# Performance work log

Measured on AMD Instinct MI355X. Metric: run time of the kernel, lower is better.

## Reference

```python
import jax, jax.numpy as jnp
import numpy as np

N_NODES = 100000
IN_CH = 256
H1, C1 = 8, 8   # conv1: heads=8, out_channels=8
H2, C2 = 1, 3   # conv2: heads=1, out_channels=3
NEG_SLOPE = 0.2
EPS = 1e-16


def gat_conv(x, src, dst, W, a_src, a_dst, b, heads, out_ch, n_nodes):
    """PyG-style GATConv (eval mode, self-loops already in src/dst)."""
    h = (x @ W).reshape(n_nodes, heads, out_ch)          # [N,H,C]
    alpha_s = jnp.einsum('nhc,hc->nh', h, a_src)         # [N,H]
    alpha_d = jnp.einsum('nhc,hc->nh', h, a_dst)         # [N,H]
    e = alpha_s[src] + alpha_d[dst]                      # [E,H]
    e = jnp.where(e > 0, e, NEG_SLOPE * e)               # leaky_relu(0.2)
    # segment softmax over destination nodes
    m = jax.ops.segment_max(e, dst, num_segments=n_nodes)
    m = jnp.where(jnp.isfinite(m), m, 0.0)
    ex = jnp.exp(e - m[dst])
    s = jax.ops.segment_sum(ex, dst, num_segments=n_nodes)
    a = ex / (s[dst] + EPS)                              # [E,H]
    msg = h[src] * a[:, :, None]                         # [E,H,C]
    out = jax.ops.segment_sum(msg, dst, num_segments=n_nodes)  # [N,H,C]
    return out.reshape(n_nodes, heads * out_ch) + b


def setup_inputs() -> dict:
    key = jax.random.key(0)
    ks = jax.random.split(key, 10)
    x = jax.random.normal(ks[0], (N_NODES, IN_CH), dtype=jnp.float32)
    edge_index = jax.random.randint(ks[1], (2, 3200000), 0, N_NODES, dtype=jnp.int64)
    sc = 0.1
    return {
        'x': x,
        'edge_index': edge_index,
        'W1': jax.random.normal(ks[2], (IN_CH, H1 * C1), dtype=jnp.float32) * sc,
        'a_src1': jax.random.normal(ks[3], (H1, C1), dtype=jnp.float32) * sc,
        'a_dst1': jax.random.normal(ks[4], (H1, C1), dtype=jnp.float32) * sc,
        'b1': jnp.zeros((H1 * C1,), dtype=jnp.float32),
        'W2': jax.random.normal(ks[5], (H1 * C1, H2 * C2), dtype=jnp.float32) * sc,
        'a_src2': jax.random.normal(ks[6], (H2, C2), dtype=jnp.float32) * sc,
        'a_dst2': jax.random.normal(ks[7], (H2, C2), dtype=jnp.float32) * sc,
        'b2': jnp.zeros((H2 * C2,), dtype=jnp.float32),
    }


def reference(x, edge_index, W1, a_src1, a_dst1, b1, W2, a_src2, a_dst2, b2):
    n = x.shape[0]
    loop = jnp.arange(n, dtype=edge_index.dtype)
    src = jnp.concatenate([edge_index[0], loop])  # add_self_loops=True
    dst = jnp.concatenate([edge_index[1], loop])
    h = gat_conv(x, src, dst, W1, a_src1, a_dst1, b1, H1, C1, n)
    h = jax.nn.elu(h)
    out = gat_conv(h, src, dst, W2, a_src2, a_dst2, b2, H2, C2, n)
    return out
```

## Files before the change

### kernel.cpp

```cpp
#include <hip/hip_runtime.h>
#include <hip/hip_bf16.h>

#define P_W1  0
#define P_AS1 16384
#define P_AD1 16448
#define P_B1  16512
#define P_W2  16576
#define P_AS2 16768
#define P_AD2 16771
#define P_B2  16774

typedef __attribute__((ext_vector_type(8))) short short8;
typedef __attribute__((ext_vector_type(4))) float floatx4;

__device__ __forceinline__ float ldf(const void* p, int i, int bf) {
  if (bf) {
    unsigned v = ((unsigned)((const unsigned short*)p)[i]) << 16;
    float f; __builtin_memcpy(&f, &v, 4); return f;
  }
  return ((const float*)p)[i];
}
__device__ __forceinline__ int ldi(const void* p, long i, int i64) {
  return i64 ? ((const int*)p)[2*i] : ((const int*)p)[i];
}
__device__ __forceinline__ unsigned short f2bfbits(float f) {
  __hip_bfloat16 b = __float2bfloat16(f);
  unsigned short u; __builtin_memcpy(&u, &b, 2); return u;
}

__global__ void k_prep(const void* x, const void* ei,
                       const void* w1, const void* as1, const void* ad1, const void* b1,
                       const void* w2, const void* as2, const void* ad2, const void* b2,
                       int* flags, float* params, unsigned short* w1t) {
  __shared__ int sh[2];
  int tid = threadIdx.x, lane = tid & 63, w = tid >> 6;
  if (w == 0) {
    const unsigned* xw = (const unsigned*)x;
    int hits = 0;
    for (int i = lane; i < 256; i += 64) {
      unsigned b = (xw[i] >> 7) & 0xFF;
      hits += (b >= 96 && b <= 141) ? 1 : 0;
    }
    for (int o = 32; o >= 1; o >>= 1) hits += __shfl_xor(hits, o);
    if (lane == 0) sh[0] = (hits >= 160) ? 1 : 0;
  } else if (w == 1) {
    const unsigned* ew = (const unsigned*)ei;
    int z = 0;
    for (int i = lane; i < 128; i += 64) z += (ew[2*i+1] == 0u) ? 1 : 0;
    for (int o = 32; o >= 1; o >>= 1) z += __shfl_xor(z, o);
    if (lane == 0) sh[1] = (z >= 64) ? 1 : 0;
  }
  __syncthreads();
  int bf = sh[0];
  if (tid == 0) { flags[0] = sh[0]; flags[1] = sh[1]; }
  for (int i = tid; i < 16384; i += blockDim.x) {
    int ch = i >> 8, k = i & 255;
    w1t[i] = f2bfbits(ldf(w1, k * 64 + ch, bf));
  }
  if (!bf) {
    for (int i = tid; i < 16384; i += blockDim.x) params[P_W1 + i] = ldf(w1, i, bf);
  }
  for (int i = tid; i < 64; i += blockDim.x) {
    params[P_AS1 + i] = ldf(as1, i, bf);
    params[P_AD1 + i] = ldf(ad1, i, bf);
    params[P_B1  + i] = ldf(b1,  i, bf);
  }
  for (int i = tid; i < 192; i += blockDim.x) params[P_W2 + i] = ldf(w2, i, bf);
  for (int i = tid; i < 3; i += blockDim.x) {
    params[P_AS2 + i] = ldf(as2, i, bf);
    params[P_AD2 + i] = ldf(ad2, i, bf);
    params[P_B2  + i] = ldf(b2,  i, bf);
  }
}

#define XP 272

__device__ __forceinline__ void gemm1_f32(const float* x, const float* params,
                                          float* h1, float* a_s, float* a_d,
                                          int N, int wave, int lane) {
  int n0 = wave * 4;
  if (n0 >= N) return;
  int nb[4];
#pragma unroll
  for (int j = 0; j < 4; j++) nb[j] = min(n0 + j, N - 1) * 256;
  float acc[4] = {0.f, 0.f, 0.f, 0.f};
  const float* W = params + P_W1;
  for (int k = 0; k < 256; k++) {
    float wv = W[k * 64 + lane];
#pragma unroll
    for (int j = 0; j < 4; j++) acc[j] += x[nb[j] + k] * wv;
  }
  float as1v = params[P_AS1 + lane], ad1v = params[P_AD1 + lane];
#pragma unroll
  for (int j = 0; j < 4; j++) {
    int n = n0 + j;
    if (n >= N) break;
    float hv = acc[j];
    float s = hv * as1v, d = hv * ad1v;
    s += __shfl_xor(s, 1); s += __shfl_xor(s, 2); s += __shfl_xor(s, 4);
    d += __shfl_xor(d, 1); d += __shfl_xor(d, 2); d += __shfl_xor(d, 4);
    h1[(size_t)n * 64 + lane] = hv;
    if ((lane & 7) == 0) {
      a_s[n * 8 + (lane >> 3)] = s;
      a_d[n * 8 + (lane >> 3)] = d;
    }
  }
}

__global__ void k_gemm1(const void* x, const unsigned short* w1t, const int* flags,
                        const float* params, float* h1, float* a_s, float* a_d, int N) {
  __shared__ unsigned short xs[16 * XP];
  int tid = threadIdx.x;
  int wv = tid >> 6, lane = tid & 63;
  if (flags[0]) {
    const unsigned short* xb = (const unsigned short*)x;
    int n0 = blockIdx.x * 16;
#pragma unroll
    for (int it = 0; it < 2; it++) {
      int idx = tid + it * 256;
      int row = idx >> 5, col = idx & 31;
      int gn = n0 + row; if (gn >= N) gn = N - 1;
      uint4 v = *(const uint4*)(xb + (size_t)gn * 256 + col * 8);
      *(uint4*)(xs + row * XP + col * 8) = v;
    }
    __syncthreads();
    int quad = lane >> 4, l16 = lane & 15;
    int ch = wv * 16 + l16;
    floatx4 acc = {0.f, 0.f, 0.f, 0.f};
    const unsigned short* xrow = xs + l16 * XP + quad * 8;
    const unsigned short* wrow = w1t + (size_t)ch * 256 + quad * 8;
#pragma unroll
    for (int k0 = 0; k0 < 256; k0 += 32) {
      short8 a = *(const short8*)(xrow + k0);
      short8 b = *(const short8*)(wrow + k0);
      acc = __builtin_amdgcn_mfma_f32_16x16x32_bf16(a, b, acc, 0, 0, 0);
    }
    float asv = params[P_AS1 + ch], adv = params[P_AD1 + ch];
#pragma unroll
    for (int r = 0; r < 4; r++) {
      int n = n0 + quad * 4 + r;
      if (n >= N) break;
      float d = acc[r];
      h1[(size_t)n * 64 + ch] = d;
      float s = d * asv, t = d * adv;
      s += __shfl_xor(s, 1); s += __shfl_xor(s, 2); s += __shfl_xor(s, 4);
      t += __shfl_xor(t, 1); t += __shfl_xor(t, 2); t += __shfl_xor(t, 4);
      if ((lane & 7) == 0) {
        int head = ch >> 3;
        a_s[n * 8 + head] = s;
        a_d[n * 8 + head] = t;
      }
    }
  } else {
    gemm1_f32((const float*)x, params, h1, a_s, a_d, N, blockIdx.x * 4 + wv, lane);
  }
}

__global__ void k_bcount(const void* ei, const int* flags, int* gcnt, int* brsv,
                         int E0, int N, int NB, int chunk) {
  __shared__ int h[256];
  int i64 = flags[1], tid = threadIdx.x;
  for (int j = tid; j < NB; j += 256) h[j] = 0;
  __syncthreads();
  int E = E0 + N;
  int b0 = blockIdx.x * chunk, b1 = min(b0 + chunk, E);
  for (int e = b0 + tid; e < b1; e += 256) {
    int dst = (e < E0) ? ldi(ei, (long)E0 + e, i64) : (e - E0);
    atomicAdd(&h[dst >> 9], 1);
  }
  __syncthreads();
  for (int j = tid; j < NB; j += 256)
    brsv[blockIdx.x * NB + j] = atomicAdd(&gcnt[j], h[j]);
}

__global__ void k_bbase(const int* gcnt, int* bbase, int NB) {
  __shared__ int sh[256];
  int tid = threadIdx.x;
  sh[tid] = (tid < NB) ? gcnt[tid] : 0;
  __syncthreads();
  int own = sh[tid];
  for (int ofs = 1; ofs < 256; ofs <<= 1) {
    int v = (tid >= ofs) ? sh[tid - ofs] : 0;
    __syncthreads();
    sh[tid] += v;
    __syncthreads();
  }
  if (tid < NB) bbase[tid] = sh[tid] - own;
  if (tid == NB - 1) bbase[NB] = sh[tid];
}

__global__ void k_bscatter(const void* ei, const int* flags, const int* bbase,
                           const int* brsv, unsigned* pairs, int E0, int N, int NB, int chunk) {
  __shared__ int base_s[256];
  __shared__ int rnk[256];
  int i64 = flags[1], tid = threadIdx.x;
  for (int j = tid; j < NB; j += 256) {
    base_s[j] = bbase[j] + brsv[blockIdx.x * NB + j];
    rnk[j] = 0;
  }
  __syncthreads();
  int E = E0 + N;
  int b0 = blockIdx.x * chunk, b1 = min(b0 + chunk, E);
  for (int e = b0 + tid; e < b1; e += 256) {
    int src, dst;
    if (e < E0) { src = ldi(ei, e, i64); dst = ldi(ei, (long)E0 + e, i64); }
    else        { src = e - E0; dst = src; }
    int bkt = dst >> 9;
    int r = atomicAdd(&rnk[bkt], 1);
    pairs[base_s[bkt] + r] = ((unsigned)src << 9) | (unsigned)(dst & 511);
  }
}

__global__ void k_bsort(const unsigned* pairs, const int* bbase, int* rowp,
                        int* srcs, int N, int NB, int E) {
  __shared__ int h0[512], sc[512], rk[512];
  int b = blockIdx.x, tid = threadIdx.x;
  int s0 = bbase[b], s1 = bbase[b + 1], L = s1 - s0;
  for (int j = tid; j < 512; j += 256) { h0[j] = 0; rk[j] = 0; }
  __syncthreads();
  for (int i = tid; i < L; i += 256) atomicAdd(&h0[pairs[s0 + i] & 511], 1);
  __syncthreads();
  for (int j = tid; j < 512; j += 256) sc[j] = h0[j];
  __syncthreads();
  for (int ofs = 1; ofs < 512; ofs <<= 1) {
    int j0 = tid, j1 = tid + 256;
    int v0 = (j0 >= ofs) ? sc[j0 - ofs] : 0;
    int v1 = (j1 >= ofs) ? sc[j1 - ofs] : 0;
    __syncthreads();
    sc[j0] += v0; sc[j1] += v1;
    __syncthreads();
  }
  for (int j = tid; j < 512; j += 256) {
    int off = sc[j] - h0[j];
    int node = (b << 9) + j;
    if (node < N) rowp[node] = s0 + off;
    sc[j] = off;
  }
  if (b == 0 && tid == 0) rowp[N] = E;
  __syncthreads();
  for (int i = tid; i < L; i += 256) {
    unsigned p = pairs[s0 + i];
    int j = p & 511;
    int r = atomicAdd(&rk[j], 1);
    srcs[s0 + sc[j] + r] = (int)(p >> 9);
  }
}

__global__ void k_agg1(const float* params, const float* h1, const float* a_s,
                       const float* a_d, const int* rowp, const int* srcs,
                       float4* pk, float* ad2, int N) {
  int n = blockIdx.x * (blockDim.x >> 6) + (threadIdx.x >> 6);
  int lane = threadIdx.x & 63;
  if (n >= N) return;
  int start = rowp[n], end = rowp[n + 1];
  int h = lane & 7, es = lane >> 3;
  float adh = a_d[n * 8 + h];
  float m = -1e30f;
  for (int i = start + es; i < end; i += 8) {
    float e = a_s[srcs[i] * 8 + h] + adh;
    e = e > 0.f ? e : 0.2f * e;
    m = fmaxf(m, e);
  }
  m = fmaxf(m, __shfl_xor(m, 8));
  m = fmaxf(m, __shfl_xor(m, 16));
  m = fmaxf(m, __shfl_xor(m, 32));
  float acc[8] = {0.f,0.f,0.f,0.f,0.f,0.f,0.f,0.f};
  float ssum = 0.f;
  for (int i = start + es; i < end; i += 8) {
    int s = srcs[i];
    float e = a_s[s * 8 + h] + adh;
    e = e > 0.f ? e : 0.2f * e;
    float ex = __expf(e - m);
    ssum += ex;
    const floatx4* hp = (const floatx4*)(h1 + (size_t)s * 64 + h * 8);
    floatx4 u0 = hp[0], u1 = hp[1];
    acc[0] += ex * u0[0]; acc[1] += ex * u0[1]; acc[2] += ex * u0[2]; acc[3] += ex * u0[3];
    acc[4] += ex * u1[0]; acc[5] += ex * u1[1]; acc[6] += ex * u1[2]; acc[7] += ex * u1[3];
  }
#pragma unroll
  for (int msk = 8; msk <= 32; msk <<= 1) {
    ssum += __shfl_xor(ssum, msk);
#pragma unroll
    for (int c = 0; c < 8; c++) acc[c] += __shfl_xor(acc[c], msk);
  }
  if (es == 0) {
    float inv = 1.f / (ssum + 1e-16f);
    float pj0 = 0.f, pj1 = 0.f, pj2 = 0.f;
#pragma unroll
    for (int c = 0; c < 8; c++) {
      float v = acc[c] * inv + params[P_B1 + h * 8 + c];
      v = v > 0.f ? v : (__expf(v) - 1.f);
      const float* w2r = params + P_W2 + (h * 8 + c) * 3;
      pj0 += v * w2r[0]; pj1 += v * w2r[1]; pj2 += v * w2r[2];
    }
    pj0 += __shfl_xor(pj0, 1); pj1 += __shfl_xor(pj1, 1); pj2 += __shfl_xor(pj2, 1);
    pj0 += __shfl_xor(pj0, 2); pj1 += __shfl_xor(pj1, 2); pj2 += __shfl_xor(pj2, 2);
    pj0 += __shfl_xor(pj0, 4); pj1 += __shfl_xor(pj1, 4); pj2 += __shfl_xor(pj2, 4);
    if (h == 0) {
      float as2 = pj0*params[P_AS2+0] + pj1*params[P_AS2+1] + pj2*params[P_AS2+2];
      float ad2v = pj0*params[P_AD2+0] + pj1*params[P_AD2+1] + pj2*params[P_AD2+2];
      pk[n] = make_float4(pj0, pj1, pj2, as2);
      ad2[n] = ad2v;
    }
  }
}

__global__ void k_agg2(const float* params, const float4* pk, const float* ad2,
                       const int* rowp, const int* srcs, void* out, const int* flags, int N) {
  int wid = blockIdx.x * (blockDim.x >> 6) + (threadIdx.x >> 6);
  int lane = threadIdx.x & 63;
  int g = lane >> 4, t = lane & 15;
  int n = wid * 4 + g;
  if (n >= N) return;
  int start = rowp[n], end = rowp[n + 1];
  float ad = ad2[n];
  float m = -1e30f;
  for (int i = start + t; i < end; i += 16) {
    float e = pk[srcs[i]].w + ad;
    e = e > 0.f ? e : 0.2f * e;
    m = fmaxf(m, e);
  }
#pragma unroll
  for (int msk = 1; msk <= 8; msk <<= 1) m = fmaxf(m, __shfl_xor(m, msk));
  float ssum = 0.f, c0 = 0.f, c1 = 0.f, c2 = 0.f;
  for (int i = start + t; i < end; i += 16) {
    float4 v = pk[srcs[i]];
    float e = v.w + ad;
    e = e > 0.f ? e : 0.2f * e;
    float ex = __expf(e - m);
    ssum += ex;
    c0 += ex * v.x; c1 += ex * v.y; c2 += ex * v.z;
  }
#pragma unroll
  for (int msk = 1; msk <= 8; msk <<= 1) {
    ssum += __shfl_xor(ssum, msk);
    c0 += __shfl_xor(c0, msk); c1 += __shfl_xor(c1, msk); c2 += __shfl_xor(c2, msk);
  }
  if (t == 0) {
    float inv = 1.f / (ssum + 1e-16f);
    float o0 = c0 * inv + params[P_B2+0];
    float o1 = c1 * inv + params[P_B2+1];
    float o2 = c2 * inv + params[P_B2+2];
    if (flags[0]) {
      __hip_bfloat16* ob = (__hip_bfloat16*)out;
      ob[n*3+0] = __float2bfloat16(o0);
      ob[n*3+1] = __float2bfloat16(o1);
      ob[n*3+2] = __float2bfloat16(o2);
    } else {
      float* of = (float*)out;
      of[n*3+0] = o0; of[n*3+1] = o1; of[n*3+2] = o2;
    }
  }
}

extern "C" void kernel_launch(void* const* d_in, const int* in_sizes, int n_in,
                              void* d_out, int out_size, void* d_ws, size_t ws_size,
                              hipStream_t stream) {
  const void* x  = d_in[0];
  const void* ei = d_in[1];
  int N  = in_sizes[0] / 256;
  int E0 = in_sizes[1] / 2;
  int E  = E0 + N;
  int NB = (N + 511) >> 9;
  const int NBLK = 512;
  int chunk = (E + NBLK - 1) / NBLK;

  char* w = (char*)d_ws;
  size_t off = 0;
  auto alloc = [&](size_t bytes) -> char* {
    char* p = w + off;
    off += (bytes + 255) & ~(size_t)255;
    return p;
  };
  int*            flags  = (int*)           alloc(256);
  float*          params = (float*)         alloc(17408 * 4);
  unsigned short* w1t    = (unsigned short*)alloc(16384 * 2);
  float*          h1     = (float*)         alloc((size_t)N * 64 * 4);
  float*          a_s1   = (float*)         alloc((size_t)N * 8 * 4);
  float*          a_d1   = (float*)         alloc((size_t)N * 8 * 4);
  float4*         pk     = (float4*)        alloc((size_t)N * 16);
  float*          ad2    = (float*)         alloc((size_t)N * 4);
  int*            gcnt   = (int*)           alloc(256 * 4);
  int*            bbase  = (int*)           alloc(257 * 4);
  int*            brsv   = (int*)           alloc((size_t)NBLK * NB * 4);
  int*            rowp   = (int*)           alloc((size_t)(N + 1) * 4);
  unsigned*       pairs  = (unsigned*)      alloc((size_t)E * 4);
  int*            srcs   = (int*)           alloc((size_t)E * 4);
  (void)ws_size; (void)n_in; (void)out_size;

  hipMemsetAsync(gcnt, 0, 256 * 4, stream);
  k_prep<<<1, 256, 0, stream>>>(x, ei, d_in[2], d_in[3], d_in[4], d_in[5],
                                d_in[6], d_in[7], d_in[8], d_in[9], flags, params, w1t);
  k_gemm1<<<dim3((N + 15) / 16), 256, 0, stream>>>(x, w1t, flags, params, h1, a_s1, a_d1, N);
  k_bcount<<<dim3(NBLK), 256, 0, stream>>>(ei, flags, gcnt, brsv, E0, N, NB, chunk);
  k_bbase<<<1, 256, 0, stream>>>(gcnt, bbase, NB);
  k_bscatter<<<dim3(NBLK), 256, 0, stream>>>(ei, flags, bbase, brsv, pairs, E0, N, NB, chunk);
  k_bsort<<<dim3(NB), 256, 0, stream>>>(pairs, bbase, rowp, srcs, N, NB, E);
  k_agg1<<<dim3((N + 3) / 4), 256, 0, stream>>>(params, h1, a_s1, a_d1, rowp, srcs, pk, ad2, N);
  k_agg2<<<dim3((N + 15) / 16), 256, 0, stream>>>(params, pk, ad2, rowp, srcs, d_out, flags, N);
}
```

Measured before the change: 728.3 us.

## Stage W1 in shared memory and compute 64-node tiles per block in gemm1

The bf16 MFMA path of the first GEMM now loads the whole transposed W1 into padded shared memory and processes 64 nodes per block. Each wave computes four 16-channel tiles, reusing each x fragment across them. The attention dot products are reduced in registers, staged in shared memory and written out coalesced, and h1 is stored as float4. The aim is to cut repeated global W1 reads and scattered small stores, at the cost of about 68KB of shared memory per block, which limits occupancy.

```diff
diff --git a/kernel.cpp b/kernel.cpp
--- a/kernel.cpp
+++ b/kernel.cpp
@@ -73,7 +73,8 @@
   }
 }
 
-#define XP 272
+#define WPAD 264
+#define XPAD 272
 
 __device__ __forceinline__ void gemm1_f32(const float* x, const float* params,
                                           float* h1, float* a_s, float* a_d,
@@ -107,52 +108,70 @@
   }
 }
 
-__global__ void k_gemm1(const void* x, const unsigned short* w1t, const int* flags,
-                        const float* params, float* h1, float* a_s, float* a_d, int N) {
-  __shared__ unsigned short xs[16 * XP];
+__global__ void __launch_bounds__(256, 2)
+k_gemm1(const void* x, const unsigned short* w1t, const int* flags,
+        const float* params, float* h1, float* a_s, float* a_d, int N) {
+  __shared__ unsigned short ws_w[64 * WPAD];
+  __shared__ unsigned short xs[64 * XPAD];
+  __shared__ float as_t[512], ad_t[512];
   int tid = threadIdx.x;
-  int wv = tid >> 6, lane = tid & 63;
+  int w = tid >> 6, lane = tid & 63;
   if (flags[0]) {
     const unsigned short* xb = (const unsigned short*)x;
-    int n0 = blockIdx.x * 16;
-#pragma unroll
-    for (int it = 0; it < 2; it++) {
-      int idx = tid + it * 256;
-      int row = idx >> 5, col = idx & 31;
-      int gn = n0 + row; if (gn >= N) gn = N - 1;
-      uint4 v = *(const uint4*)(xb + (size_t)gn * 256 + col * 8);
-      *(uint4*)(xs + row * XP + col * 8) = v;
+    int n0 = blockIdx.x * 64;
+#pragma unroll
+    for (int j = 0; j < 8; j++) {
+      int c = tid + j * 256;
+      int r = c >> 5, col = c & 31;
+      uint4 wv4 = *(const uint4*)(w1t + (size_t)r * 256 + col * 8);
+      *(uint4*)(ws_w + r * WPAD + col * 8) = wv4;
+      int gn = n0 + r; if (gn >= N) gn = N - 1;
+      uint4 xv4 = *(const uint4*)(xb + (size_t)gn * 256 + col * 8);
+      *(uint4*)(xs + r * XPAD + col * 8) = xv4;
     }
     __syncthreads();
     int quad = lane >> 4, l16 = lane & 15;
-    int ch = wv * 16 + l16;
-    floatx4 acc = {0.f, 0.f, 0.f, 0.f};
-    const unsigned short* xrow = xs + l16 * XP + quad * 8;
-    const unsigned short* wrow = w1t + (size_t)ch * 256 + quad * 8;
+    floatx4 acc[4] = {{0,0,0,0},{0,0,0,0},{0,0,0,0},{0,0,0,0}};
+    const unsigned short* xrow = xs + (w * 16 + l16) * XPAD + quad * 8;
+    const unsigned short* wr0 = ws_w + l16 * WPAD + quad * 8;
 #pragma unroll
     for (int k0 = 0; k0 < 256; k0 += 32) {
-      short8 a = *(const short8*)(xrow + k0);
-      short8 b = *(const short8*)(wrow + k0);
-      acc = __builtin_amdgcn_mfma_f32_16x16x32_bf16(a, b, acc, 0, 0, 0);
-    }
-    float asv = params[P_AS1 + ch], adv = params[P_AD1 + ch];
-#pragma unroll
-    for (int r = 0; r < 4; r++) {
-      int n = n0 + quad * 4 + r;
-      if (n >= N) break;
-      float d = acc[r];
-      h1[(size_t)n * 64 + ch] = d;
-      float s = d * asv, t = d * adv;
-      s += __shfl_xor(s, 1); s += __shfl_xor(s, 2); s += __shfl_xor(s, 4);
-      t += __shfl_xor(t, 1); t += __shfl_xor(t, 2); t += __shfl_xor(t, 4);
-      if ((lane & 7) == 0) {
-        int head = ch >> 3;
-        a_s[n * 8 + head] = s;
-        a_d[n * 8 + head] = t;
+      short8 bx = *(const short8*)(xrow + k0);
+#pragma unroll
+      for (int ct = 0; ct < 4; ct++) {
+        short8 aw = *(const short8*)(wr0 + ct * 16 * WPAD + k0);
+        acc[ct] = __builtin_amdgcn_mfma_f32_16x16x32_bf16(aw, bx, acc[ct], 0, 0, 0);
       }
     }
+    int n = n0 + w * 16 + l16;
+    bool nv = n < N;
+#pragma unroll
+    for (int ct = 0; ct < 4; ct++) {
+      int chb = ct * 16 + quad * 4;
+      float4 dv = make_float4(acc[ct][0], acc[ct][1], acc[ct][2], acc[ct][3]);
+      if (nv) *(float4*)(h1 + (size_t)n * 64 + chb) = dv;
+      float sp = dv.x * params[P_AS1+chb] + dv.y * params[P_AS1+chb+1]
+               + dv.z * params[P_AS1+chb+2] + dv.w * params[P_AS1+chb+3];
+      float dp = dv.x * params[P_AD1+chb] + dv.y * params[P_AD1+chb+1]
+               + dv.z * params[P_AD1+chb+2] + dv.w * params[P_AD1+chb+3];
+      sp += __shfl_xor(sp, 16);
+      dp += __shfl_xor(dp, 16);
+      if ((quad & 1) == 0) {
+        int head = ct * 2 + (quad >> 1);
+        as_t[(w * 16 + l16) * 8 + head] = sp;
+        ad_t[(w * 16 + l16) * 8 + head] = dp;
+      }
+    }
+    __syncthreads();
+    for (int t = tid; t < 512; t += 256) {
+      int n2 = n0 + (t >> 3);
+      if (n2 < N) { a_s[n0 * 8 + t] = as_t[t]; a_d[n0 * 8 + t] = ad_t[t]; }
+    }
   } else {
-    gemm1_f32((const float*)x, params, h1, a_s, a_d, N, blockIdx.x * 4 + wv, lane);
+#pragma unroll
+    for (int j = 0; j < 4; j++)
+      gemm1_f32((const float*)x, params, h1, a_s, a_d, N,
+                blockIdx.x * 16 + j * 4 + w, lane);
   }
 }
 
@@ -391,7 +410,7 @@
   hipMemsetAsync(gcnt, 0, 256 * 4, stream);
   k_prep<<<1, 256, 0, stream>>>(x, ei, d_in[2], d_in[3], d_in[4], d_in[5],
                                 d_in[6], d_in[7], d_in[8], d_in[9], flags, params, w1t);
-  k_gemm1<<<dim3((N + 15) / 16), 256, 0, stream>>>(x, w1t, flags, params, h1, a_s1, a_d1, N);
+  k_gemm1<<<dim3((N + 63) / 64), 256, 0, stream>>>(x, w1t, flags, params, h1, a_s1, a_d1, N);
   k_bcount<<<dim3(NBLK), 256, 0, stream>>>(ei, flags, gcnt, brsv, E0, N, NB, chunk);
   k_bbase<<<1, 256, 0, stream>>>(gcnt, bbase, NB);
   k_bscatter<<<dim3(NBLK), 256, 0, stream>>>(ei, flags, bbase, brsv, pairs, E0, N, NB, chunk);
```

After: 784.3 us. 7.7% more time.
